# Kernel optimization log

Measured on AMD Instinct MI355X. Metric: run time of the kernel, lower is better.

The kernel has to match this reference:

```python
import jax, jax.numpy as jnp
import numpy as np
import math

OMEGA_0 = 30.0
LAYER_SIZES = [3, 256, 256, 256, 256, 3]
N_POINTS = 524288


def _siren_params(key):
    """SIREN initialization matching the original module."""
    keys = jax.random.split(key, len(LAYER_SIZES) - 1)
    params = {}
    for i in range(len(LAYER_SIZES) - 1):
        in_dim, out_dim = LAYER_SIZES[i], LAYER_SIZES[i + 1]
        k = keys[i]
        bound = (1.0 / in_dim) if i == 0 else (math.sqrt(6.0 / in_dim) / OMEGA_0)
        W = jax.random.uniform(k, (out_dim, in_dim), minval=-bound, maxval=bound, dtype=jnp.float32)
        b = jax.random.uniform(k, (out_dim,), minval=-1e-6, maxval=1e-6, dtype=jnp.float32)
        params[f"W{i}"] = W
        params[f"b{i}"] = b
    return params


def setup_inputs() -> dict:
    key = jax.random.key(0)
    kx, kp = jax.random.split(key)
    # coordinates in [-1, 1], typical SIREN input domain
    x = jax.random.uniform(kx, (N_POINTS, 3), minval=-1.0, maxval=1.0, dtype=jnp.float32)
    inp = {"x": x}
    inp.update(_siren_params(kp))
    return inp


def reference(x, W0, b0, W1, b1, W2, b2, W3, b3, W4, b4):
    # First layer: sin(omega_0 * (W0 @ x + b0)), batched over rows of x.
    h = jnp.sin(OMEGA_0 * (jnp.einsum("ni,oi->no", x, W0) + b0))
    # Hidden layers: sin(W @ h + b)
    h = jnp.sin(jnp.einsum("ni,oi->no", h, W1) + b1)
    h = jnp.sin(jnp.einsum("ni,oi->no", h, W2) + b2)
    h = jnp.sin(jnp.einsum("ni,oi->no", h, W3) + b3)
    # Final layer: linear, no activation.
    out = jnp.einsum("ni,oi->no", h, W4) + b4
    return out
```

## Files before the change

kernel.cpp:

```cpp
#include <hip/hip_runtime.h>
#include <stdint.h>


typedef float    f32x4 __attribute__((ext_vector_type(4)));
typedef short    s16x8 __attribute__((ext_vector_type(8)));
typedef uint32_t u32x2 __attribute__((ext_vector_type(2)));
typedef uint32_t u32x4 __attribute__((ext_vector_type(4)));

#define INV2PI 0.15915494309189535f
#define L0SCALE 4.774648292756860f
#define W4OFF 196608

__device__ __forceinline__ uint32_t pack_bf16x2(float lo, float hi) {
#if __has_builtin(__builtin_amdgcn_cvt_pk_bf16_f32)
    auto v = __builtin_amdgcn_cvt_pk_bf16_f32(lo, hi);
    return __builtin_bit_cast(uint32_t, v);
#else
    uint32_t a = __builtin_bit_cast(uint32_t, lo);
    uint32_t b = __builtin_bit_cast(uint32_t, hi);
    a += 0x7FFFu + ((a >> 16) & 1u);
    b += 0x7FFFu + ((b >> 16) & 1u);
    return (a >> 16) | (b & 0xFFFF0000u);
#endif
}
__device__ __forceinline__ float sin_rev(float r) {
    return __builtin_amdgcn_sinf(r);
}

__global__ void convert_weights(const float* __restrict__ W1,
                                const float* __restrict__ W2,
                                const float* __restrict__ W3,
                                const float* __restrict__ W4,
                                uint16_t* __restrict__ wsb) {
    int u = blockIdx.x * blockDim.x + threadIdx.x;
    if (u < 24576) {
        int n16 = u & 15, q = (u >> 4) & 3, cH = (u >> 6) & 15,
            kc = (u >> 10) & 7, l = u >> 13;
        const float* W = (l == 0) ? W1 : (l == 1) ? W2 : W3;
        const float* src = W + (cH * 16 + n16) * 256 + kc * 32 + q * 8;
        u32x4 pk;
        #pragma unroll
        for (int j2 = 0; j2 < 4; ++j2)
            pk[j2] = pack_bf16x2(src[2 * j2] * INV2PI, src[2 * j2 + 1] * INV2PI);
        *(u32x4*)(wsb + u * 8) = pk;
    } else if (u < 25088) {
        int e = u - 24576;
        int lane = e & 63, kc = e >> 6;
        int n16 = lane & 15, q = lane >> 4;
        u32x4 pk = { 0u, 0u, 0u, 0u };
        if (n16 < 3) {
            const float* src = W4 + n16 * 256 + kc * 32 + q * 8;
            #pragma unroll
            for (int j2 = 0; j2 < 4; ++j2)
                pk[j2] = pack_bf16x2(src[2 * j2], src[2 * j2 + 1]);
        }
        *(u32x4*)(wsb + W4OFF + e * 8) = pk;
    }
}

__global__ __launch_bounds__(256, 2) void siren_main(
    const float* __restrict__ x,
    const float* __restrict__ W0, const float* __restrict__ b0,
    const float* __restrict__ b1, const float* __restrict__ b2,
    const float* __restrict__ b3,
    const float* __restrict__ b4,
    const uint16_t* __restrict__ Wb,
    float* __restrict__ out)
{
    __shared__ uint16_t h_lds[4096 * 8];

    const int tid  = threadIdx.x;
    const int lane = tid & 63;
    const int wid  = tid >> 6;
    const int n16  = lane & 15;
    const int q    = lane >> 4;
    const int p0   = blockIdx.x * 128;

    {
        float xv[8][3];
        #pragma unroll
        for (int rt = 0; rt < 8; ++rt) {
            const float* xp = x + (p0 + rt * 16 + n16) * 3;
            xv[rt][0] = xp[0]; xv[rt][1] = xp[1]; xv[rt][2] = xp[2];
        }
        #pragma unroll
        for (int oo = 0; oo < 2; ++oo) {
            const int octet = wid * 8 + oo * 4 + q;
            const float* w0r = W0 + octet * 24;
            float wv[24];
            #pragma unroll
            for (int i = 0; i < 24; ++i) wv[i] = w0r[i] * L0SCALE;
            float bb[8];
            #pragma unroll
            for (int i = 0; i < 8; ++i) bb[i] = b0[octet * 8 + i] * L0SCALE;
            const int kc0 = octet >> 2, q0 = octet & 3;
            #pragma unroll
            for (int rt = 0; rt < 8; ++rt) {
                u32x4 pk;
                #pragma unroll
                for (int j2 = 0; j2 < 4; ++j2) {
                    float za = wv[(2*j2  )*3+0] * xv[rt][0] +
                               wv[(2*j2  )*3+1] * xv[rt][1] +
                               wv[(2*j2  )*3+2] * xv[rt][2] + bb[2*j2];
                    float zb = wv[(2*j2+1)*3+0] * xv[rt][0] +
                               wv[(2*j2+1)*3+1] * xv[rt][1] +
                               wv[(2*j2+1)*3+2] * xv[rt][2] + bb[2*j2+1];
                    pk[j2] = pack_bf16x2(sin_rev(za), sin_rev(zb));
                }
                *(u32x4*)&h_lds[((kc0 * 8 + rt) * 64 + q0 * 16 + n16) * 8] = pk;
            }
        }
    }
    __syncthreads();

    #pragma unroll
    for (int l = 0; l < 3; ++l) {
        const uint16_t* wsl = Wb + l * 65536;
        const float* bl = (l == 0) ? b1 : (l == 1) ? b2 : b3;

        s16x8 Wbuf[2][4];
        #pragma unroll
        for (int t = 0; t < 4; ++t)
            Wbuf[0][t] = *(const s16x8*)(wsl + ((wid * 4 + t) * 64 + lane) * 8);

        f32x4 acc[4][8];
        #pragma unroll
        for (int t = 0; t < 4; ++t) {
            f32x4 bv = *(const f32x4*)&bl[wid * 64 + t * 16 + q * 4];
            bv *= INV2PI;
            #pragma unroll
            for (int pt = 0; pt < 8; ++pt) acc[t][pt] = bv;
        }

        #pragma unroll
        for (int kc = 0; kc < 8; ++kc) {
            const int cur = kc & 1, nxt = cur ^ 1;
            if (kc < 7) {
                #pragma unroll
                for (int t = 0; t < 4; ++t)
                    Wbuf[nxt][t] = *(const s16x8*)(wsl +
                        (((kc + 1) * 16 + wid * 4 + t) * 64 + lane) * 8);
            }
            {
                s16x8 hf[4];
                #pragma unroll
                for (int pt = 0; pt < 4; ++pt)
                    hf[pt] = *(const s16x8*)&h_lds[((kc * 8 + pt) * 64 + lane) * 8];
                #pragma unroll
                for (int t = 0; t < 4; ++t)
                    #pragma unroll
                    for (int pt = 0; pt < 4; ++pt)
                        acc[t][pt] = __builtin_amdgcn_mfma_f32_16x16x32_bf16(
                            Wbuf[cur][t], hf[pt], acc[t][pt], 0, 0, 0);
            }
            {
                s16x8 hf[4];
                #pragma unroll
                for (int pt = 0; pt < 4; ++pt)
                    hf[pt] = *(const s16x8*)&h_lds[((kc * 8 + 4 + pt) * 64 + lane) * 8];
                #pragma unroll
                for (int t = 0; t < 4; ++t)
                    #pragma unroll
                    for (int pt = 0; pt < 4; ++pt)
                        acc[t][4 + pt] = __builtin_amdgcn_mfma_f32_16x16x32_bf16(
                            Wbuf[cur][t], hf[pt], acc[t][4 + pt], 0, 0, 0);
            }
        }
        __syncthreads();

        uint32_t* hw = (uint32_t*)h_lds;
        #pragma unroll
        for (int t = 0; t < 4; ++t) {
            const int kcp = wid * 2 + (t >> 1);
            const int qp  = (t * 2 + (q >> 1)) & 3;
            #pragma unroll
            for (int pt = 0; pt < 8; ++pt) {
                float s0 = sin_rev(acc[t][pt][0]);
                float s1 = sin_rev(acc[t][pt][1]);
                float s2 = sin_rev(acc[t][pt][2]);
                float s3 = sin_rev(acc[t][pt][3]);
                int base = ((kcp * 8 + pt) * 64 + qp * 16 + n16) * 4 + (q & 1) * 2;
                u32x2 w2 = { pack_bf16x2(s0, s1), pack_bf16x2(s2, s3) };
                *(u32x2*)&hw[base] = w2;
            }
        }
        __syncthreads();
    }

    {
        float bb4 = (n16 < 3) ? b4[n16] : 0.0f;
        f32x4 accF[2] = { { bb4, bb4, bb4, bb4 }, { bb4, bb4, bb4, bb4 } };
        #pragma unroll
        for (int kc = 0; kc < 8; ++kc) {
            s16x8 w4f = *(const s16x8*)(Wb + W4OFF + (kc * 64 + lane) * 8);
            #pragma unroll
            for (int hh = 0; hh < 2; ++hh) {
                s16x8 af = *(const s16x8*)&h_lds[
                    ((kc * 8 + wid * 2 + hh) * 64 + lane) * 8];
                accF[hh] = __builtin_amdgcn_mfma_f32_16x16x32_bf16(
                    af, w4f, accF[hh], 0, 0, 0);
            }
        }
        if (n16 < 3) {
            #pragma unroll
            for (int hh = 0; hh < 2; ++hh)
                #pragma unroll
                for (int r = 0; r < 4; ++r)
                    out[(p0 + (wid * 2 + hh) * 16 + q * 4 + r) * 3 + n16] = accF[hh][r];
        }
    }
}

extern "C" void kernel_launch(void* const* d_in, const int* in_sizes, int n_in,
                              void* d_out, int out_size, void* d_ws, size_t ws_size,
                              hipStream_t stream) {
    const float* x  = (const float*)d_in[0];
    const float* W0 = (const float*)d_in[1];
    const float* b0 = (const float*)d_in[2];
    const float* W1 = (const float*)d_in[3];
    const float* b1 = (const float*)d_in[4];
    const float* W2 = (const float*)d_in[5];
    const float* b2 = (const float*)d_in[6];
    const float* W3 = (const float*)d_in[7];
    const float* b3 = (const float*)d_in[8];
    const float* W4 = (const float*)d_in[9];
    const float* b4 = (const float*)d_in[10];
    float* outp     = (float*)d_out;
    uint16_t* wsb   = (uint16_t*)d_ws;

    hipLaunchKernelGGL(convert_weights, dim3(98), dim3(256), 0, stream,
                       W1, W2, W3, W4, wsb);
    hipLaunchKernelGGL(siren_main, dim3(4096), dim3(256), 0, stream,
                       x, W0, b0, b1, b2, b3, b4, wsb, outp);
}
```

Before: 278.3 us.

## Split hidden-layer GEMM into 2x2 wave grid over output channels and points

Each wave used to compute 64 output channels across all 128 points. It now computes 128 channels across 64 points, with the four waves arranged 2x2 by channel half and point half. Each wave reads half as many LDS activation fragments and twice as many global weight fragments per k-chunk. The explicit double-buffered weight prefetch is dropped, so the weight loads, which are L2-resident, are no longer software-pipelined ahead of the MFMAs and may expose latency.

```diff
diff --git a/kernel.cpp b/kernel.cpp
--- a/kernel.cpp
+++ b/kernel.cpp
@@ -72,6 +72,8 @@
     const int tid  = threadIdx.x;
     const int lane = tid & 63;
     const int wid  = tid >> 6;
+    const int cw   = wid & 1;
+    const int pw   = wid >> 1;
     const int n16  = lane & 15;
     const int q    = lane >> 4;
     const int p0   = blockIdx.x * 128;
@@ -118,68 +120,64 @@
         const uint16_t* wsl = Wb + l * 65536;
         const float* bl = (l == 0) ? b1 : (l == 1) ? b2 : b3;
 
-        s16x8 Wbuf[2][4];
-        #pragma unroll
-        for (int t = 0; t < 4; ++t)
-            Wbuf[0][t] = *(const s16x8*)(wsl + ((wid * 4 + t) * 64 + lane) * 8);
-
-        f32x4 acc[4][8];
-        #pragma unroll
-        for (int t = 0; t < 4; ++t) {
-            f32x4 bv = *(const f32x4*)&bl[wid * 64 + t * 16 + q * 4];
+        f32x4 acc[8][4];
+        #pragma unroll
+        for (int t = 0; t < 8; ++t) {
+            f32x4 bv = *(const f32x4*)&bl[cw * 128 + t * 16 + q * 4];
             bv *= INV2PI;
             #pragma unroll
-            for (int pt = 0; pt < 8; ++pt) acc[t][pt] = bv;
+            for (int pt = 0; pt < 4; ++pt) acc[t][pt] = bv;
         }
 
         #pragma unroll
         for (int kc = 0; kc < 8; ++kc) {
-            const int cur = kc & 1, nxt = cur ^ 1;
-            if (kc < 7) {
-                #pragma unroll
-                for (int t = 0; t < 4; ++t)
-                    Wbuf[nxt][t] = *(const s16x8*)(wsl +
-                        (((kc + 1) * 16 + wid * 4 + t) * 64 + lane) * 8);
-            }
+            s16x8 hf[4];
+            #pragma unroll
+            for (int pt = 0; pt < 4; ++pt)
+                hf[pt] = *(const s16x8*)&h_lds[
+                    ((kc * 8 + pw * 4 + pt) * 64 + lane) * 8];
             {
-                s16x8 hf[4];
-                #pragma unroll
-                for (int pt = 0; pt < 4; ++pt)
-                    hf[pt] = *(const s16x8*)&h_lds[((kc * 8 + pt) * 64 + lane) * 8];
+                s16x8 wf[4];
+                #pragma unroll
+                for (int t = 0; t < 4; ++t)
+                    wf[t] = *(const s16x8*)(wsl +
+                        ((kc * 16 + cw * 8 + t) * 64 + lane) * 8);
                 #pragma unroll
                 for (int t = 0; t < 4; ++t)
                     #pragma unroll
                     for (int pt = 0; pt < 4; ++pt)
                         acc[t][pt] = __builtin_amdgcn_mfma_f32_16x16x32_bf16(
-                            Wbuf[cur][t], hf[pt], acc[t][pt], 0, 0, 0);
+                            wf[t], hf[pt], acc[t][pt], 0, 0, 0);
             }
             {
-                s16x8 hf[4];
-                #pragma unroll
-                for (int pt = 0; pt < 4; ++pt)
-                    hf[pt] = *(const s16x8*)&h_lds[((kc * 8 + 4 + pt) * 64 + lane) * 8];
+                s16x8 wf[4];
+                #pragma unroll
+                for (int t = 0; t < 4; ++t)
+                    wf[t] = *(const s16x8*)(wsl +
+                        ((kc * 16 + cw * 8 + 4 + t) * 64 + lane) * 8);
                 #pragma unroll
                 for (int t = 0; t < 4; ++t)
                     #pragma unroll
                     for (int pt = 0; pt < 4; ++pt)
-                        acc[t][4 + pt] = __builtin_amdgcn_mfma_f32_16x16x32_bf16(
-                            Wbuf[cur][t], hf[pt], acc[t][4 + pt], 0, 0, 0);
+                        acc[4 + t][pt] = __builtin_amdgcn_mfma_f32_16x16x32_bf16(
+                            wf[t], hf[pt], acc[4 + t][pt], 0, 0, 0);
             }
         }
         __syncthreads();
 
         uint32_t* hw = (uint32_t*)h_lds;
         #pragma unroll
-        for (int t = 0; t < 4; ++t) {
-            const int kcp = wid * 2 + (t >> 1);
-            const int qp  = (t * 2 + (q >> 1)) & 3;
-            #pragma unroll
-            for (int pt = 0; pt < 8; ++pt) {
+        for (int t = 0; t < 8; ++t) {
+            const int kcp = cw * 4 + (t >> 1);
+            const int qp  = (t & 1) * 2 + (q >> 1);
+            #pragma unroll
+            for (int pt = 0; pt < 4; ++pt) {
                 float s0 = sin_rev(acc[t][pt][0]);
                 float s1 = sin_rev(acc[t][pt][1]);
                 float s2 = sin_rev(acc[t][pt][2]);
                 float s3 = sin_rev(acc[t][pt][3]);
-                int base = ((kcp * 8 + pt) * 64 + qp * 16 + n16) * 4 + (q & 1) * 2;
+                int base = ((kcp * 8 + pw * 4 + pt) * 64 + qp * 16 + n16) * 4
+                           + (q & 1) * 2;
                 u32x2 w2 = { pack_bf16x2(s0, s1), pack_bf16x2(s2, s3) };
                 *(u32x2*)&hw[base] = w2;
             }
```

After: 387.2 us. +39.1%, slower.
